# Kernel tuning notes

Measured on AMD Instinct MI355X. Metric: run time of the kernel, lower is better.

## Reference

```python
import jax, jax.numpy as jnp
import numpy as np

N, P, C, S, H, CLS = 32, 16, 256, 128, 4, 3000
DH = C // H
EPS = 1e-5


def setup_inputs() -> dict:
    key = jax.random.key(0)
    ks = jax.random.split(key, 8)
    sh = (N, P, C, S)
    return {
        "t_f": jax.random.normal(ks[0], sh, jnp.float32),
        "t_s": jax.random.normal(ks[1], sh, jnp.float32),
        "t_l": jax.random.normal(ks[2], sh, jnp.float32),
        # grouped 1x1 conv weights, one [out_ch, in_ch] matrix per part
        "decay_w": jax.random.normal(ks[3], (P, C, 3 * C), jnp.float32) * 0.02,
        "qkv_w": jax.random.normal(ks[4], (P, 3 * C, C), jnp.float32) * 0.02,
        "out_w": jax.random.normal(ks[5], (P, C, C), jnp.float32) * 0.02,
        # per-part BatchNorm1d affine params
        "gamma": jnp.ones((P, C), jnp.float32),
        "beta": jnp.zeros((P, C), jnp.float32),
        # classifier fc: [in_planes, class_num] (broadcast over parts)
        "fc": jax.random.normal(ks[6], (C, CLS), jnp.float32) * 0.02,
    }


def reference(t_f, t_s, t_l, decay_w, qkv_w, out_w, gamma, beta, fc):
    n, p, c, s = t_f.shape
    h, dh = H, DH
    scale = dh ** -0.5

    # decay_c: grouped 1x1 conv, 3c -> c per part
    x_cat = jnp.concatenate([t_f, t_s, t_l], axis=2)            # [n,p,3c,s]
    t_all = jnp.einsum('npis,poi->npos', x_cat, decay_w)        # [n,p,c,s]

    # Attention.to_qkv: grouped 1x1 conv, c -> 3c per part
    qkv = jnp.einsum('npcs,pqc->npqs', t_all, qkv_w)            # [n,p,3c,s]
    qkv = qkv.reshape(n, p, 3, h, dh, s).transpose(2, 0, 3, 1, 4, 5)  # [3,n,h,p,dh,s]
    q, k, v = qkv[0], qkv[1], qkv[2]

    # frame-frame attention per (head, part): [n,h,p,s,s]
    dots = jnp.einsum('nhpcs,nhpct->nhpst', q, k) * scale
    attn = jax.nn.softmax(dots, axis=-1)

    o = jnp.einsum('nhpst,nhpct->nhpcs', attn, v)               # [n,h,p,dh,s]
    o = o.transpose(0, 2, 1, 3, 4).reshape(n, p, c, s)          # [n,p,c,s]
    o = jnp.einsum('npcs,poc->npos', o, out_w)                  # to_out grouped conv

    # residual + max over frames
    wpv = (o + t_all).max(axis=-1)                              # [n,p,c]

    # select_topk_part (topk_num == 1 forced by squeeze(2) in torch code):
    # argmax over frames of column-summed attention, gather that frame of t_f, sum heads
    idx = jnp.argmax(attn.sum(axis=-2), axis=-1)                # [n,h,p]
    ib = jnp.broadcast_to(idx[:, :, :, None, None], (n, h, p, c, 1))
    sel = jnp.take_along_axis(t_f[:, None], ib, axis=-1)[..., 0]  # [n,h,p,c]
    sel = sel.sum(axis=1)                                       # [n,p,c]

    # per-part BatchNorm1d in training mode (batch statistics over n)
    mean = wpv.mean(axis=0)                                     # [p,c]
    var = wpv.var(axis=0)                                       # biased, as torch BN
    pf = (wpv - mean) / jnp.sqrt(var + EPS) * gamma + beta      # [n,p,c]

    cls = jnp.einsum('npc,ck->npk', pf, fc)                     # [n,p,class_num]
    return cls, wpv.transpose(1, 0, 2), sel.transpose(1, 0, 2)
```

## Files before the change

kernel.cpp:

```cpp
#include <hip/hip_runtime.h>
#include <math.h>

#define N_ 32
#define P_ 16
#define C_ 256
#define S_ 128
#define H_ 4
#define CLS_ 3000

typedef __attribute__((ext_vector_type(4))) float f4v;
typedef __attribute__((ext_vector_type(4))) float f32x4;
typedef __attribute__((ext_vector_type(8))) short short8;
typedef __attribute__((ext_vector_type(4))) unsigned short us4;

__device__ __forceinline__ unsigned short f2bf(float x){
    unsigned u = __float_as_uint(x);
    u += 0x7fffu + ((u >> 16) & 1u);
    return (unsigned short)(u >> 16);
}
__device__ __forceinline__ float bf2f(unsigned short h){
    return __uint_as_float(((unsigned)h) << 16);
}

typedef __attribute__((address_space(1))) const unsigned int gu32_t;
typedef __attribute__((address_space(3))) unsigned int lu32_t;
__device__ __forceinline__ void gload16(const void* g, void* l){
    __builtin_amdgcn_global_load_lds((gu32_t*)g, (lu32_t*)l, 16, 0, 0);
}

__global__ void wsplit(const float* __restrict__ dw, const float* __restrict__ qw,
                       const float* __restrict__ ow,
                       unsigned short* __restrict__ wdh, unsigned short* __restrict__ wdl,
                       unsigned short* __restrict__ wqh, unsigned short* __restrict__ wql,
                       unsigned short* __restrict__ woh){
    int i = blockIdx.x * 256 + threadIdx.x;
    int stride = gridDim.x * 256;
    for (; i < 3145728; i += stride){
        float a = dw[i]; unsigned short h = f2bf(a);
        wdh[i] = h; wdl[i] = f2bf(a - bf2f(h));
        float b = qw[i]; unsigned short h2 = f2bf(b);
        wqh[i] = h2; wql[i] = f2bf(b - bf2f(h2));
        if (i < 1048576) woh[i] = f2bf(ow[i]);
    }
}

__global__ __launch_bounds__(256) void fct_kernel(const float* __restrict__ fc,
                                                  unsigned short* __restrict__ fcT){
    int n = blockIdx.x * 256 + threadIdx.x;
    if (n < CLS_){
        for (int c = 0; c < 256; ++c) fcT[(size_t)n * 256 + c] = f2bf(fc[(size_t)c * CLS_ + n]);
    } else {
        for (int c = 0; c < 256; ++c) fcT[(size_t)n * 256 + c] = 0;
    }
}

__global__ __launch_bounds__(256) void gemm0t(
    const float* __restrict__ t_f, const float* __restrict__ t_s,
    const float* __restrict__ t_l,
    const unsigned short* __restrict__ Whi, const unsigned short* __restrict__ Wlo,
    unsigned short* __restrict__ outH, unsigned short* __restrict__ outL,
    int n0, int cnp)
{
    __shared__ unsigned short sm[24576];
    float* Tf = (float*)sm;
    unsigned short* AhL = sm + 8192;
    unsigned short* AlL = sm + 12288;
    unsigned short* BhL = sm + 16384;
    unsigned short* BlL = sm + 20480;
    unsigned short* Ep  = sm;

    const int id = blockIdx.x;
    const int xcd = id & 7;
    const int r = id >> 3;
    const int ppl = r / (cnp * 2);
    const int rr = r % (cnp * 2);
    const int n_l = rr >> 1;
    const int o_t = rr & 1;
    const int p = xcd * 2 + ppl;
    const int np_l = n_l * 16 + p;
    const int o0 = o_t * 128;
    const size_t np_g = (size_t)(n0 + n_l) * 16 + p;

    const int tid = threadIdx.x;
    const int w = tid >> 6, l = tid & 63;
    const int lr = l & 15, lg = l >> 4;
    const int ws0 = (w & 1) * 64, wo0 = (w >> 1) * 64;
    const int s2 = tid & 127, khalf = tid >> 7;

    const unsigned short* Wp_h = Whi + ((size_t)p * 256 + o0) * 768;
    const unsigned short* Wp_l = Wlo + ((size_t)p * 256 + o0) * 768;

    f32x4 acc[4][4];
#pragma unroll
    for (int i = 0; i < 4; ++i)
#pragma unroll
        for (int j = 0; j < 4; ++j) acc[i][j] = (f32x4){0.f, 0.f, 0.f, 0.f};

    for (int k0 = 0; k0 < 768; k0 += 32){
        const int t = k0 >> 8;
        const float* src = (t == 0) ? t_f : ((t == 1) ? t_s : t_l);
        const float* xbase = src + (np_g * 256 + (k0 & 255)) * 128;
#pragma unroll
        for (int it = 0; it < 4; ++it){
            int lin = (w * 4 + it) * 64 + l;
            gload16(xbase + lin * 4, Tf + lin * 4);
        }
#pragma unroll
        for (int it = 0; it < 2; ++it){
            int lin = (w * 2 + it) * 64 + l;
            int row = lin >> 2, ch = lin & 3;
            int sk = ((ch ^ ((row >> 1) & 3)) << 3);
            gload16(Wp_h + (size_t)row * 768 + k0 + sk, BhL + lin * 8);
            gload16(Wp_l + (size_t)row * 768 + k0 + sk, BlL + lin * 8);
        }
        __syncthreads();
        {
            short8 h0, h1, l0, l1;
#pragma unroll
            for (int j = 0; j < 8; ++j){
                float v = Tf[(khalf * 16 + j) * 128 + s2];
                unsigned short hh = f2bf(v);
                h0[j] = (short)hh; l0[j] = (short)f2bf(v - bf2f(hh));
            }
#pragma unroll
            for (int j = 0; j < 8; ++j){
                float v = Tf[(khalf * 16 + 8 + j) * 128 + s2];
                unsigned short hh = f2bf(v);
                h1[j] = (short)hh; l1[j] = (short)f2bf(v - bf2f(hh));
            }
            int sb = (s2 >> 1) & 3;
            int c0 = (khalf * 2) ^ sb, c1 = (khalf * 2 + 1) ^ sb;
            *(short8*)(AhL + s2 * 32 + c0 * 8) = h0;
            *(short8*)(AhL + s2 * 32 + c1 * 8) = h1;
            *(short8*)(AlL + s2 * 32 + c0 * 8) = l0;
            *(short8*)(AlL + s2 * 32 + c1 * 8) = l1;
        }
        __syncthreads();
        short8 ah[4], al[4];
#pragma unroll
        for (int sf = 0; sf < 4; ++sf){
            int row = ws0 + sf * 16 + lr;
            int cof = (lg ^ ((row >> 1) & 3)) << 3;
            ah[sf] = *(const short8*)(AhL + row * 32 + cof);
            al[sf] = *(const short8*)(AlL + row * 32 + cof);
        }
#pragma unroll
        for (int of = 0; of < 4; ++of){
            int row = wo0 + of * 16 + lr;
            int cof = (lg ^ ((row >> 1) & 3)) << 3;
            short8 bh = *(const short8*)(BhL + row * 32 + cof);
            short8 bl = *(const short8*)(BlL + row * 32 + cof);
#pragma unroll
            for (int sf = 0; sf < 4; ++sf){
                acc[sf][of] = __builtin_amdgcn_mfma_f32_16x16x32_bf16(ah[sf], bh, acc[sf][of], 0, 0, 0);
                acc[sf][of] = __builtin_amdgcn_mfma_f32_16x16x32_bf16(ah[sf], bl, acc[sf][of], 0, 0, 0);
                acc[sf][of] = __builtin_amdgcn_mfma_f32_16x16x32_bf16(al[sf], bh, acc[sf][of], 0, 0, 0);
            }
        }
        __syncthreads();
    }

#pragma unroll
    for (int plane = 0; plane < 2; ++plane){
#pragma unroll
        for (int sf = 0; sf < 4; ++sf)
#pragma unroll
            for (int of = 0; of < 4; ++of){
                int col = wo0 + of * 16 + lr;
#pragma unroll
                for (int r2 = 0; r2 < 4; ++r2){
                    int row = ws0 + sf * 16 + lg * 4 + r2;
                    float v = acc[sf][of][r2];
                    unsigned short hh = f2bf(v);
                    unsigned short q = plane ? f2bf(v - bf2f(hh)) : hh;
                    Ep[row * 136 + col] = q;
                }
            }
        __syncthreads();
        unsigned short* dst = plane ? outL : outH;
#pragma unroll
        for (int it = 0; it < 8; ++it){
            int idx = tid + 256 * it;
            int row = idx >> 4, seg = (idx & 15) * 8;
            *(short8*)(dst + (size_t)np_l * 128 * 256 + (size_t)row * 256 + o0 + seg) =
                *(const short8*)(Ep + row * 136 + seg);
        }
        __syncthreads();
    }
}

template<int KEXT, int APITCH, int ND, int MODE, int OPITCH>
__global__ __launch_bounds__(256) void gemm3(
    const unsigned short* __restrict__ Ah_g, const unsigned short* __restrict__ Al_g,
    const unsigned short* __restrict__ Whi, const unsigned short* __restrict__ Wlo,
    const unsigned short* __restrict__ resH, const unsigned short* __restrict__ resL,
    unsigned short* __restrict__ outH, unsigned short* __restrict__ outL,
    float* __restrict__ outF, int n0, int cnp)
{
    constexpr int T3 = (MODE == 2) ? 0 : 1;
    constexpr int OB = ND / 128;
    constexpr int BUFSH = T3 ? 16384 : 8192;
    __shared__ unsigned short sm[2 * BUFSH];
    unsigned short* Ep = sm;
    __shared__ float cmax[2][2][64];

    const int id = blockIdx.x;
    const int xcd = id & 7;
    const int r = id >> 3;
    const int ppl = r / (cnp * OB);
    const int rr = r % (cnp * OB);
    const int n_l = rr / OB;
    const int o_t = rr % OB;
    const int p = xcd * 2 + ppl;
    const int np_l = n_l * 16 + p;
    const int o0 = o_t * 128;

    const int tid = threadIdx.x;
    const int w = tid >> 6, l = tid & 63;
    const int lr = l & 15, lg = l >> 4;
    const int ws0 = (w & 1) * 64, wo0 = (w >> 1) * 64;
    const size_t aBase = (size_t)np_l * 128 * APITCH;
    const unsigned short* Wp_h = Whi + ((size_t)p * ND + o0) * KEXT;
    const unsigned short* Wp_l = T3 ? (Wlo + ((size_t)p * ND + o0) * KEXT) : Wp_h;

    f32x4 acc[4][4];
#pragma unroll
    for (int i = 0; i < 4; ++i)
#pragma unroll
        for (int j = 0; j < 4; ++j) acc[i][j] = (f32x4){0.f, 0.f, 0.f, 0.f};

    auto STAGE = [&](int bsel, int k0){
        unsigned short* B0 = sm + bsel * BUFSH;
#pragma unroll
        for (int it = 0; it < 2; ++it){
            int slot = w * 2 + it;
            int lin = slot * 64 + l;
            int row = lin >> 2, ch = lin & 3;
            int sk = ((ch ^ ((row >> 1) & 3)) << 3);
            gload16(Ah_g + aBase + (size_t)row * APITCH + k0 + sk, B0 + slot * 512);
            gload16(Wp_h + (size_t)row * KEXT + k0 + sk, B0 + 4096 + slot * 512);
            if (T3){
                gload16(Al_g + aBase + (size_t)row * APITCH + k0 + sk, B0 + 8192 + slot * 512);
                gload16(Wp_l + (size_t)row * KEXT + k0 + sk, B0 + 12288 + slot * 512);
            }
        }
    };

    STAGE(0, 0);
    __syncthreads();
    int cur = 0;
    for (int k0 = 0; k0 < KEXT; k0 += 32){
        if (k0 + 32 < KEXT) STAGE(cur ^ 1, k0 + 32);
        unsigned short* AhL = sm + cur * BUFSH;
        unsigned short* BhL = AhL + 4096;
        unsigned short* AlL = T3 ? (AhL + 8192) : AhL;
        unsigned short* BlL = T3 ? (AhL + 12288) : AhL;
        short8 ah[4], al[4];
#pragma unroll
        for (int sf = 0; sf < 4; ++sf){
            int row = ws0 + sf * 16 + lr;
            int cof = (lg ^ ((row >> 1) & 3)) << 3;
            ah[sf] = *(const short8*)(AhL + row * 32 + cof);
            if (T3) al[sf] = *(const short8*)(AlL + row * 32 + cof);
        }
#pragma unroll
        for (int of = 0; of < 4; ++of){
            int row = wo0 + of * 16 + lr;
            int cof = (lg ^ ((row >> 1) & 3)) << 3;
            short8 bh = *(const short8*)(BhL + row * 32 + cof);
            short8 bl = bh;
            if (T3) bl = *(const short8*)(BlL + row * 32 + cof);
#pragma unroll
            for (int sf = 0; sf < 4; ++sf){
                acc[sf][of] = __builtin_amdgcn_mfma_f32_16x16x32_bf16(ah[sf], bh, acc[sf][of], 0, 0, 0);
                if (T3){
                    acc[sf][of] = __builtin_amdgcn_mfma_f32_16x16x32_bf16(ah[sf], bl, acc[sf][of], 0, 0, 0);
                    acc[sf][of] = __builtin_amdgcn_mfma_f32_16x16x32_bf16(al[sf], bh, acc[sf][of], 0, 0, 0);
                }
            }
        }
        __syncthreads();
        cur ^= 1;
    }

    if (MODE != 2){
#pragma unroll
        for (int plane = 0; plane < 2; ++plane){
#pragma unroll
            for (int sf = 0; sf < 4; ++sf)
#pragma unroll
                for (int of = 0; of < 4; ++of){
                    int col = wo0 + of * 16 + lr;
#pragma unroll
                    for (int r2 = 0; r2 < 4; ++r2){
                        int row = ws0 + sf * 16 + lg * 4 + r2;
                        float v = acc[sf][of][r2];
                        unsigned short hh = f2bf(v);
                        unsigned short q = plane ? f2bf(v - bf2f(hh)) : hh;
                        Ep[row * 136 + col] = q;
                    }
                }
            __syncthreads();
            unsigned short* dst = plane ? outL : outH;
#pragma unroll
            for (int it = 0; it < 8; ++it){
                int idx = tid + 256 * it;
                int row = idx >> 4, seg = (idx & 15) * 8;
                *(short8*)(dst + (size_t)np_l * 128 * OPITCH + (size_t)row * OPITCH + o0 + seg) =
                    *(const short8*)(Ep + row * 136 + seg);
            }
            __syncthreads();
        }
    } else {
        const int n_g = n0 + n_l;
#pragma unroll
        for (int of = 0; of < 4; ++of){
            int oc = o0 + wo0 + of * 16 + lr;
            float m = -INFINITY;
#pragma unroll
            for (int sf = 0; sf < 4; ++sf){
#pragma unroll
                for (int r2 = 0; r2 < 4; ++r2){
                    int s = ws0 + sf * 16 + lg * 4 + r2;
                    size_t ri = (size_t)np_l * 128 * 256 + (size_t)s * 256 + oc;
                    float v = acc[sf][of][r2] + bf2f(resH[ri]) + bf2f(resL[ri]);
                    m = fmaxf(m, v);
                }
            }
            m = fmaxf(m, __shfl_xor(m, 16));
            m = fmaxf(m, __shfl_xor(m, 32));
            if (l < 16) cmax[w >> 1][w & 1][of * 16 + l] = m;
        }
        __syncthreads();
        if (tid < 128){
            int oh = tid >> 6, col = tid & 63;
            float v = fmaxf(cmax[oh][0][col], cmax[oh][1][col]);
            outF[((size_t)p * N_ + n_g) * C_ + o0 + oh * 64 + col] = v;
        }
    }
}

__global__ __launch_bounds__(256) void attn3(unsigned short* __restrict__ qH,
                                             const unsigned short* __restrict__ qL,
                                             int* __restrict__ idxA, int n0, int cnp){
    __shared__ char smraw[17408 + 34816 + 2048];
    unsigned short* Vs = (unsigned short*)smraw;
    unsigned short* Pm = (unsigned short*)(smraw + 17408);
    float* csW = (float*)(smraw + 17408 + 34816);
    unsigned short* Ot = (unsigned short*)smraw;

    const int id = blockIdx.x;
    const int xcd = id & 7;
    const int r = id >> 3;
    const int ppl = r / (cnp * 4);
    const int rr = r % (cnp * 4);
    const int n_l = rr >> 2, h = rr & 3;
    const int p = xcd * 2 + ppl;
    const int np_l = n_l * 16 + p;
    const int tid = threadIdx.x, w = tid >> 6, l = tid & 63;
    const int lr = l & 15, lg = l >> 4;
    unsigned short* baseH = qH + (size_t)np_l * 128 * 768;
    const unsigned short* baseL = qL + (size_t)np_l * 128 * 768;

#pragma unroll
    for (int it = 0; it < 8; ++it){
        int idx = tid + 256 * it;
        int t = idx >> 4, d4 = (idx & 15) * 4;
        us4 v = *(const us4*)(baseH + (size_t)t * 768 + 512 + h * 64 + d4);
#pragma unroll
        for (int j = 0; j < 4; ++j) Vs[(d4 + j) * 136 + t] = v[j];
    }

    short8 qh[2][2], ql[2][2];
#pragma unroll
    for (int sf = 0; sf < 2; ++sf)
#pragma unroll
        for (int ks = 0; ks < 2; ++ks){
            size_t off = (size_t)(w * 32 + sf * 16 + lr) * 768 + h * 64 + ks * 32 + lg * 8;
            qh[sf][ks] = *(const short8*)(baseH + off);
            ql[sf][ks] = *(const short8*)(baseL + off);
        }

    f32x4 dacc[2][8];
#pragma unroll
    for (int i = 0; i < 2; ++i)
#pragma unroll
        for (int j = 0; j < 8; ++j) dacc[i][j] = (f32x4){0.f, 0.f, 0.f, 0.f};

#pragma unroll
    for (int tf = 0; tf < 8; ++tf){
#pragma unroll
        for (int ks = 0; ks < 2; ++ks){
            size_t off = (size_t)(tf * 16 + lr) * 768 + 256 + h * 64 + ks * 32 + lg * 8;
            short8 kh = *(const short8*)(baseH + off);
            short8 kl = *(const short8*)(baseL + off);
#pragma unroll
            for (int sf = 0; sf < 2; ++sf){
                dacc[sf][tf] = __builtin_amdgcn_mfma_f32_16x16x32_bf16(qh[sf][ks], kh, dacc[sf][tf], 0, 0, 0);
                dacc[sf][tf] = __builtin_amdgcn_mfma_f32_16x16x32_bf16(qh[sf][ks], kl, dacc[sf][tf], 0, 0, 0);
                dacc[sf][tf] = __builtin_amdgcn_mfma_f32_16x16x32_bf16(ql[sf][ks], kh, dacc[sf][tf], 0, 0, 0);
            }
        }
    }

    float csp[8];
#pragma unroll
    for (int tf = 0; tf < 8; ++tf) csp[tf] = 0.f;
#pragma unroll
    for (int sf = 0; sf < 2; ++sf){
#pragma unroll
        for (int r2 = 0; r2 < 4; ++r2){
            float m = -INFINITY;
#pragma unroll
            for (int tf = 0; tf < 8; ++tf) m = fmaxf(m, dacc[sf][tf][r2]);
            m = fmaxf(m, __shfl_xor(m, 1)); m = fmaxf(m, __shfl_xor(m, 2));
            m = fmaxf(m, __shfl_xor(m, 4)); m = fmaxf(m, __shfl_xor(m, 8));
            float e[8]; float sum = 0.f;
#pragma unroll
            for (int tf = 0; tf < 8; ++tf){
                e[tf] = __expf(0.125f * (dacc[sf][tf][r2] - m)); sum += e[tf];
            }
            sum += __shfl_xor(sum, 1); sum += __shfl_xor(sum, 2);
            sum += __shfl_xor(sum, 4); sum += __shfl_xor(sum, 8);
            float inv = 1.f / sum;
            int s = w * 32 + sf * 16 + lg * 4 + r2;
#pragma unroll
            for (int tf = 0; tf < 8; ++tf){
                float pv = e[tf] * inv;
                Pm[s * 136 + tf * 16 + lr] = f2bf(pv);
                csp[tf] += pv;
            }
        }
    }
#pragma unroll
    for (int tf = 0; tf < 8; ++tf){
        float v = csp[tf];
        v += __shfl_xor(v, 16); v += __shfl_xor(v, 32);
        if (l < 16) csW[w * 128 + tf * 16 + l] = v;
    }
    __syncthreads();

    f32x4 oacc[8];
#pragma unroll
    for (int i = 0; i < 8; ++i) oacc[i] = (f32x4){0.f, 0.f, 0.f, 0.f};
#pragma unroll
    for (int ks = 0; ks < 4; ++ks){
        short8 av = *(const short8*)(Vs + (w * 16 + lr) * 136 + ks * 32 + lg * 8);
#pragma unroll
        for (int sf = 0; sf < 8; ++sf){
            short8 bp = *(const short8*)(Pm + (sf * 16 + lr) * 136 + ks * 32 + lg * 8);
            oacc[sf] = __builtin_amdgcn_mfma_f32_16x16x32_bf16(av, bp, oacc[sf], 0, 0, 0);
        }
    }
    __syncthreads();

    if (tid < 64){
        float v0 = csW[tid] + csW[128 + tid] + csW[256 + tid] + csW[384 + tid];
        float v1 = csW[64 + tid] + csW[192 + tid] + csW[320 + tid] + csW[448 + tid];
        float bv; int bi;
        if (v1 > v0){ bv = v1; bi = 64 + tid; } else { bv = v0; bi = tid; }
#pragma unroll
        for (int msk = 1; msk <= 32; msk <<= 1){
            float ov = __shfl_xor(bv, msk); int oi = __shfl_xor(bi, msk);
            if (ov > bv || (ov == bv && oi < bi)){ bv = ov; bi = oi; }
        }
        if (tid == 0){ int n_g = n0 + n_l; idxA[(n_g * H_ + h) * P_ + p] = bi; }
    }

#pragma unroll
    for (int sf = 0; sf < 8; ++sf){
        int s = sf * 16 + lr;
#pragma unroll
        for (int r2 = 0; r2 < 4; ++r2) Ot[s * 72 + w * 16 + lg * 4 + r2] = f2bf(oacc[sf][r2]);
    }
    __syncthreads();
#pragma unroll
    for (int it = 0; it < 4; ++it){
        int idx = tid + 256 * it;
        int s = idx >> 3, d8 = (idx & 7) * 8;
        *(short8*)(baseH + (size_t)s * 768 + h * 64 + d8) = *(const short8*)(Ot + s * 72 + d8);
    }
}

__global__ void bn_stats(const float* __restrict__ wpvT,
                         const float* __restrict__ gamma,
                         const float* __restrict__ beta,
                         float* __restrict__ aArr, float* __restrict__ bArr)
{
    int i = blockIdx.x * blockDim.x + threadIdx.x;
    if (i >= P_ * C_) return;
    int p = i / C_, c = i % C_;
    const float* basep = wpvT + (size_t)p * N_ * C_ + c;
    float su = 0.f, s2 = 0.f;
    for (int n = 0; n < N_; ++n){
        float v = basep[n * C_];
        su += v; s2 += v * v;
    }
    float mean = su * (1.f / N_);
    float var = s2 * (1.f / N_) - mean * mean;
    float rstd = rsqrtf(var + 1e-5f);
    float a = gamma[i] * rstd;
    aArr[i] = a;
    bArr[i] = beta[i] - mean * a;
}

__global__ __launch_bounds__(256) void pf_kernel(const float* __restrict__ wpvT,
                                                 const float* __restrict__ aArr,
                                                 const float* __restrict__ bArr,
                                                 unsigned short* __restrict__ pfb){
    int m = blockIdx.x, c = threadIdx.x;
    int p = m >> 5;
    float v = wpvT[(size_t)m * 256 + c];
    pfb[(size_t)m * 256 + c] = f2bf(v * aArr[p * 256 + c] + bArr[p * 256 + c]);
}

__global__ __launch_bounds__(256) void gemmc(const unsigned short* __restrict__ pfb,
                                             const unsigned short* __restrict__ fcT,
                                             float* __restrict__ cls){
    __shared__ unsigned short sm[2 * 128 * 72];
    unsigned short* AhL = sm;
    unsigned short* BhL = sm + 128 * 72;

    const int tid = threadIdx.x;
    const int w = tid >> 6, l = tid & 63;
    const int lr = l & 15, lg = l >> 4;
    const int ws0 = (w & 1) * 64, wo0 = (w >> 1) * 64;
    const int o0 = blockIdx.x * 128;
    const int m0 = blockIdx.y * 128;

    f32x4 acc[4][4];
#pragma unroll
    for (int i = 0; i < 4; ++i)
#pragma unroll
        for (int j = 0; j < 4; ++j) acc[i][j] = (f32x4){0.f, 0.f, 0.f, 0.f};

    for (int k0 = 0; k0 < 256; k0 += 64){
#pragma unroll
        for (int it = 0; it < 4; ++it){
            int idx = tid + 256 * it;
            int s = idx >> 3, c8 = (idx & 7) * 8;
            *(short8*)(AhL + s * 72 + c8) = *(const short8*)(pfb + (size_t)(m0 + s) * 256 + k0 + c8);
            *(short8*)(BhL + s * 72 + c8) = *(const short8*)(fcT + (size_t)(o0 + s) * 256 + k0 + c8);
        }
        __syncthreads();
#pragma unroll
        for (int ks = 0; ks < 2; ++ks){
            short8 ah[4];
#pragma unroll
            for (int sf = 0; sf < 4; ++sf)
                ah[sf] = *(const short8*)(AhL + (ws0 + sf * 16 + lr) * 72 + ks * 32 + lg * 8);
#pragma unroll
            for (int of = 0; of < 4; ++of){
                short8 bh = *(const short8*)(BhL + (wo0 + of * 16 + lr) * 72 + ks * 32 + lg * 8);
#pragma unroll
                for (int sf = 0; sf < 4; ++sf)
                    acc[sf][of] = __builtin_amdgcn_mfma_f32_16x16x32_bf16(ah[sf], bh, acc[sf][of], 0, 0, 0);
            }
        }
        __syncthreads();
    }
#pragma unroll
    for (int sf = 0; sf < 4; ++sf)
#pragma unroll
        for (int of = 0; of < 4; ++of){
            int oc = o0 + wo0 + of * 16 + lr;
            if (oc < CLS_){
#pragma unroll
                for (int r2 = 0; r2 < 4; ++r2){
                    int m = m0 + ws0 + sf * 16 + lg * 4 + r2;
                    int n = m & 31, p = m >> 5;
                    cls[((size_t)n * 16 + p) * CLS_ + oc] = acc[sf][of][r2];
                }
            }
        }
}

__global__ void sel_kernel(const float* __restrict__ t_f,
                           const int* __restrict__ idxArr,
                           float* __restrict__ selT)
{
    const int np = blockIdx.x;
    const int n = np >> 4, p = np & 15;
    const int c = threadIdx.x;
    float acc = 0.f;
#pragma unroll
    for (int h = 0; h < H_; ++h){
        int s = idxArr[(n * H_ + h) * P_ + p];
        acc += t_f[((size_t)np * C_ + c) * S_ + s];
    }
    selT[((size_t)p * N_ + n) * C_ + c] = acc;
}

extern "C" void kernel_launch(void* const* d_in, const int* in_sizes, int n_in,
                              void* d_out, int out_size, void* d_ws, size_t ws_size,
                              hipStream_t stream)
{
    const float* t_f     = (const float*)d_in[0];
    const float* t_s     = (const float*)d_in[1];
    const float* t_l     = (const float*)d_in[2];
    const float* decay_w = (const float*)d_in[3];
    const float* qkv_w   = (const float*)d_in[4];
    const float* out_w   = (const float*)d_in[5];
    const float* gamma   = (const float*)d_in[6];
    const float* beta    = (const float*)d_in[7];
    const float* fc      = (const float*)d_in[8];
    float* out = (float*)d_out;

    const size_t WD = 3145728, WQ = 3145728, WO = 1048576;
    char* basep = (char*)d_ws;
    unsigned short* wdh = (unsigned short*)basep;
    unsigned short* wdl = wdh + WD;
    unsigned short* wqh = wdl + WD;
    unsigned short* wql = wqh + WQ;
    unsigned short* woh = wql + WQ;
    unsigned short* fcT = woh + WO;
    unsigned short* pfb = fcT + 3072 * 256;
    float* aArr = (float*)(pfb + 512 * 256);
    float* bArr = aArr + P_ * C_;
    int* idxA = (int*)(bArr + P_ * C_);
    char* big = (char*)(idxA + N_ * H_ * P_);
    size_t head = (size_t)(big - basep);
    size_t avail = (ws_size > head) ? (ws_size - head) : 0;
    const size_t per_n = (size_t)16 * 128 * (256 + 768) * 2 * 2;
    int cn = (int)(avail / per_n);
    if (cn < 1) cn = 1;
    if (cn > N_) cn = N_;
    int nch = (N_ + cn - 1) / cn;
    cn = (N_ + nch - 1) / nch;

    unsigned short* tH = (unsigned short*)big;
    unsigned short* tL = tH + (size_t)cn * 16 * 128 * 256;
    unsigned short* qH = tL + (size_t)cn * 16 * 128 * 256;
    unsigned short* qL = qH + (size_t)cn * 16 * 128 * 768;

    float* cls  = out;
    float* wpvT = out + (size_t)N_ * P_ * CLS_;
    float* selT = wpvT + (size_t)P_ * N_ * C_;

    wsplit<<<2048, 256, 0, stream>>>(decay_w, qkv_w, out_w, wdh, wdl, wqh, wql, woh);
    fct_kernel<<<12, 256, 0, stream>>>(fc, fcT);

    for (int n0 = 0; n0 < N_; n0 += cn){
        int c = (N_ - n0 < cn) ? (N_ - n0) : cn;
        int npg = c * 16;
        gemm0t<<<npg * 2, 256, 0, stream>>>(
            t_f, t_s, t_l, wdh, wdl, tH, tL, n0, c);
        gemm3<256, 256, 768, 1, 768><<<npg * 6, 256, 0, stream>>>(
            tH, tL, wqh, wql, nullptr, nullptr, qH, qL, nullptr, n0, c);
        attn3<<<c * 64, 256, 0, stream>>>(qH, qL, idxA, n0, c);
        gemm3<256, 768, 256, 2, 256><<<npg * 2, 256, 0, stream>>>(
            qH, qH, woh, woh, tH, tL, nullptr, nullptr, wpvT, n0, c);
    }
    bn_stats<<<(P_ * C_ + 255) / 256, 256, 0, stream>>>(wpvT, gamma, beta, aArr, bArr);
    pf_kernel<<<512, 256, 0, stream>>>(wpvT, aArr, bArr, pfb);
    gemmc<<<dim3(24, 4), 256, 0, stream>>>(pfb, fcT, cls);
    sel_kernel<<<N_ * P_, 256, 0, stream>>>(t_f, idxA, selT);
}
```

Baseline: 448.1 us.

## Single-buffer gemm3 LDS staging and split out-projection into narrower output tiles

The double-buffered LDS staging in gemm3 becomes a single buffer, with a barrier after each load. This shrinks shared memory per block (the qkv variant drops from 64 KB to about 34 KB), which lets more blocks reside per CU. A new TOB template parameter sets the output tile width: the out-projection/max-reduction launch uses 64-wide tiles and twice as many blocks, while the qkv launch stays at 128. The cost is that global loads no longer overlap MFMA work within a block, and the out-projection re-reads its A tile once per extra block.

```diff
diff --git a/kernel.cpp b/kernel.cpp
--- a/kernel.cpp
+++ b/kernel.cpp
@@ -189,7 +189,7 @@
     }
 }
 
-template<int KEXT, int APITCH, int ND, int MODE, int OPITCH>
+template<int KEXT, int APITCH, int ND, int MODE, int OPITCH, int TOB>
 __global__ __launch_bounds__(256) void gemm3(
     const unsigned short* __restrict__ Ah_g, const unsigned short* __restrict__ Al_g,
     const unsigned short* __restrict__ Whi, const unsigned short* __restrict__ Wlo,
@@ -198,9 +198,13 @@
     float* __restrict__ outF, int n0, int cnp)
 {
     constexpr int T3 = (MODE == 2) ? 0 : 1;
-    constexpr int OB = ND / 128;
-    constexpr int BUFSH = T3 ? 16384 : 8192;
-    __shared__ unsigned short sm[2 * BUFSH];
+    constexpr int OB = ND / TOB;
+    constexpr int OF = TOB / 32;
+    __shared__ unsigned short sm[T3 ? 17408 : (4096 + TOB * 32)];
+    unsigned short* AhL = sm;
+    unsigned short* BhL = sm + 4096;
+    unsigned short* AlL = T3 ? (sm + 8192) : sm;
+    unsigned short* BlL = T3 ? (sm + 12288) : sm;
     unsigned short* Ep = sm;
     __shared__ float cmax[2][2][64];
 
@@ -213,48 +217,44 @@
     const int o_t = rr % OB;
     const int p = xcd * 2 + ppl;
     const int np_l = n_l * 16 + p;
-    const int o0 = o_t * 128;
+    const int o0 = o_t * TOB;
 
     const int tid = threadIdx.x;
     const int w = tid >> 6, l = tid & 63;
     const int lr = l & 15, lg = l >> 4;
-    const int ws0 = (w & 1) * 64, wo0 = (w >> 1) * 64;
+    const int ws0 = (w & 1) * 64, wo0 = (w >> 1) * (TOB / 2);
     const size_t aBase = (size_t)np_l * 128 * APITCH;
     const unsigned short* Wp_h = Whi + ((size_t)p * ND + o0) * KEXT;
     const unsigned short* Wp_l = T3 ? (Wlo + ((size_t)p * ND + o0) * KEXT) : Wp_h;
 
-    f32x4 acc[4][4];
+    f32x4 acc[4][OF];
 #pragma unroll
     for (int i = 0; i < 4; ++i)
 #pragma unroll
-        for (int j = 0; j < 4; ++j) acc[i][j] = (f32x4){0.f, 0.f, 0.f, 0.f};
-
-    auto STAGE = [&](int bsel, int k0){
-        unsigned short* B0 = sm + bsel * BUFSH;
+        for (int j = 0; j < OF; ++j) acc[i][j] = (f32x4){0.f, 0.f, 0.f, 0.f};
+
+    for (int k0 = 0; k0 < KEXT; k0 += 32){
 #pragma unroll
         for (int it = 0; it < 2; ++it){
             int slot = w * 2 + it;
             int lin = slot * 64 + l;
             int row = lin >> 2, ch = lin & 3;
             int sk = ((ch ^ ((row >> 1) & 3)) << 3);
-            gload16(Ah_g + aBase + (size_t)row * APITCH + k0 + sk, B0 + slot * 512);
-            gload16(Wp_h + (size_t)row * KEXT + k0 + sk, B0 + 4096 + slot * 512);
-            if (T3){
-                gload16(Al_g + aBase + (size_t)row * APITCH + k0 + sk, B0 + 8192 + slot * 512);
-                gload16(Wp_l + (size_t)row * KEXT + k0 + sk, B0 + 12288 + slot * 512);
-            }
-        }
-    };
-
-    STAGE(0, 0);
-    __syncthreads();
-    int cur = 0;
-    for (int k0 = 0; k0 < KEXT; k0 += 32){
-        if (k0 + 32 < KEXT) STAGE(cur ^ 1, k0 + 32);
-        unsigned short* AhL = sm + cur * BUFSH;
-        unsigned short* BhL = AhL + 4096;
-        unsigned short* AlL = T3 ? (AhL + 8192) : AhL;
-        unsigned short* BlL = T3 ? (AhL + 12288) : AhL;
+            gload16(Ah_g + aBase + (size_t)row * APITCH + k0 + sk, AhL + slot * 512);
+            if (T3)
+                gload16(Al_g + aBase + (size_t)row * APITCH + k0 + sk, AlL + slot * 512);
+        }
+#pragma unroll
+        for (int it = 0; it < TOB / 64; ++it){
+            int slot = w * (TOB / 64) + it;
+            int lin = slot * 64 + l;
+            int row = lin >> 2, ch = lin & 3;
+            int sk = ((ch ^ ((row >> 1) & 3)) << 3);
+            gload16(Wp_h + (size_t)row * KEXT + k0 + sk, BhL + slot * 512);
+            if (T3)
+                gload16(Wp_l + (size_t)row * KEXT + k0 + sk, BlL + slot * 512);
+        }
+        __syncthreads();
         short8 ah[4], al[4];
 #pragma unroll
         for (int sf = 0; sf < 4; ++sf){
@@ -264,7 +264,7 @@
             if (T3) al[sf] = *(const short8*)(AlL + row * 32 + cof);
         }
 #pragma unroll
-        for (int of = 0; of < 4; ++of){
+        for (int of = 0; of < OF; ++of){
             int row = wo0 + of * 16 + lr;
             int cof = (lg ^ ((row >> 1) & 3)) << 3;
             short8 bh = *(const short8*)(BhL + row * 32 + cof);
@@ -280,7 +280,6 @@
             }
         }
         __syncthreads();
-        cur ^= 1;
     }
 
     if (MODE != 2){
@@ -289,7 +288,7 @@
 #pragma unroll
             for (int sf = 0; sf < 4; ++sf)
 #pragma unroll
-                for (int of = 0; of < 4; ++of){
+                for (int of = 0; of < OF; ++of){
                     int col = wo0 + of * 16 + lr;
 #pragma unroll
                     for (int r2 = 0; r2 < 4; ++r2){
@@ -314,7 +313,7 @@
     } else {
         const int n_g = n0 + n_l;
 #pragma unroll
-        for (int of = 0; of < 4; ++of){
+        for (int of = 0; of < OF; ++of){
             int oc = o0 + wo0 + of * 16 + lr;
             float m = -INFINITY;
 #pragma unroll
@@ -332,10 +331,10 @@
             if (l < 16) cmax[w >> 1][w & 1][of * 16 + l] = m;
         }
         __syncthreads();
-        if (tid < 128){
-            int oh = tid >> 6, col = tid & 63;
+        if (tid < TOB){
+            int oh = tid >> 5, col = tid & 31;
             float v = fmaxf(cmax[oh][0][col], cmax[oh][1][col]);
-            outF[((size_t)p * N_ + n_g) * C_ + o0 + oh * 64 + col] = v;
+            outF[((size_t)p * N_ + n_g) * C_ + o0 + oh * 32 + col] = v;
         }
     }
 }
@@ -645,10 +644,10 @@
         int npg = c * 16;
         gemm0t<<<npg * 2, 256, 0, stream>>>(
             t_f, t_s, t_l, wdh, wdl, tH, tL, n0, c);
-        gemm3<256, 256, 768, 1, 768><<<npg * 6, 256, 0, stream>>>(
+        gemm3<256, 256, 768, 1, 768, 128><<<npg * 6, 256, 0, stream>>>(
             tH, tL, wqh, wql, nullptr, nullptr, qH, qL, nullptr, n0, c);
         attn3<<<c * 64, 256, 0, stream>>>(qH, qL, idxA, n0, c);
-        gemm3<256, 768, 256, 2, 256><<<npg * 2, 256, 0, stream>>>(
+        gemm3<256, 768, 256, 2, 256, 64><<<npg * 4, 256, 0, stream>>>(
             qH, qH, woh, woh, tH, tL, nullptr, nullptr, wpvT, n0, c);
     }
     bn_stats<<<(P_ * C_ + 255) / 256, 256, 0, stream>>>(wpvT, gamma, beta, aArr, bArr);
```

Measured after the change: 443.7 us. Within noise of the previous version (-1.0%).
